# Kernel optimization log

Measured on AMD Instinct MI355X. Metric: run time of the kernel, lower is better.

## Reference

```python
import jax, jax.numpy as jnp
import numpy as np

B, T, S1, S2 = 4, 256, 256, 256
D = 512          # tgt_dims == src_dims
V = 32000        # tgt_voc_size
H, DH = 8, 64    # heads, head_dims; HID = H*DH == D
HID = H * DH
VEXT = V + S1 + S2


def layer_norm(x):
    m = jnp.mean(x, axis=-1, keepdims=True)
    v = jnp.mean((x - m) ** 2, axis=-1, keepdims=True)
    return (x - m) / jnp.sqrt(v + 1e-5)


def copy_attention(query, key, qmask, kmask, Wq, bq, Wk, bk, Wv, bv, Wo, bo):
    # conv1d with kernel 1 == linear; weights are [out, in]
    b, t, _ = query.shape
    s = key.shape[1]
    q = (query @ Wq.T + bq).reshape(b, t, H, DH).transpose(0, 2, 1, 3) * (DH ** -0.5)
    k = (key @ Wk.T + bk).reshape(b, s, H, DH).transpose(0, 2, 1, 3)
    v = (key @ Wv.T + bv).reshape(b, s, H, DH).transpose(0, 2, 1, 3)
    att = jnp.einsum('bhtd,bhkd->bhtk', q, k)            # [B,H,T,S]
    out_att = att * kmask[:, None, None, :]              # multiplicative mask copy
    att = jnp.where((kmask == 0)[:, None, None, :], -jnp.inf, att)
    att = jax.nn.softmax(att, axis=-1)
    out = jnp.einsum('bhtk,bhkd->bhtd', att, v)
    out = out.transpose(0, 2, 1, 3).reshape(b, t, HID)
    out = (out @ Wo.T + bo) * qmask[:, :, None]
    out_att = out_att * qmask[:, None, :, None]
    return out_att.mean(axis=1), out                     # [B,T,S], [B,T,D]


def scatter_copy(att, map_idx):
    # copy_output[b, t, map_idx[b, s]] += att[b, t, s]  (accumulate=True)
    b, t, s = att.shape
    bi = jnp.arange(b)[:, None, None]
    ti = jnp.arange(t)[None, :, None]
    out = jnp.zeros((b, t, VEXT), att.dtype)
    return out.at[bi, ti, map_idx[:, None, :]].add(att)


def setup_inputs() -> dict:
    key = jax.random.key(0)
    ks = jax.random.split(key, 24)
    p = 0.02
    inp = {
        'tgt_dec_out': jax.random.normal(ks[0], (B, T, D), jnp.float32),
        'src1_key': jax.random.normal(ks[1], (B, S1, D), jnp.float32),
        'src1_map_idx': jax.random.randint(ks[2], (B, S1), 0, VEXT),
        'src2_key': jax.random.normal(ks[3], (B, S2, D), jnp.float32),
        'src2_map_idx': jax.random.randint(ks[4], (B, S2), 0, VEXT),
        'Wfc': jax.random.normal(ks[5], (V, D), jnp.float32) * p,
        'bfc': jnp.zeros((V,), jnp.float32),
        'Wp': jax.random.normal(ks[6], (3, 3 * D), jnp.float32) * p,
        'bp': jnp.zeros((3,), jnp.float32),
    }
    i = 7
    for a in ('1', '2'):
        for nm in ('Wq', 'Wk', 'Wv', 'Wo'):
            inp[nm + a] = jax.random.normal(ks[i], (HID, D), jnp.float32) * p
            inp[nm.replace('W', 'b') + a] = jnp.zeros((HID,), jnp.float32)
            i += 1
    return inp


def reference(tgt_dec_out, src1_key, src1_map_idx, src2_key, src2_map_idx,
              Wfc, bfc, Wp, bp,
              Wq1, bq1, Wk1, bk1, Wv1, bv1, Wo1, bo1,
              Wq2, bq2, Wk2, bk2, Wv2, bv2, Wo2, bo2):
    tgt_output = layer_norm(tgt_dec_out @ Wfc.T + bfc)          # [B,T,V]
    tgt_output = jnp.pad(tgt_output, ((0, 0), (0, 0), (0, S1 + S2)))  # [B,T,VEXT]
    tgt_mask = jnp.sign(jnp.abs(tgt_dec_out).sum(-1))
    src1_mask = jnp.sign(jnp.abs(src1_key).sum(-1))
    src2_mask = jnp.sign(jnp.abs(src2_key).sum(-1))
    att1, c1 = copy_attention(tgt_dec_out, src1_key, tgt_mask, src1_mask,
                              Wq1, bq1, Wk1, bk1, Wv1, bv1, Wo1, bo1)
    copy1 = scatter_copy(layer_norm(att1), src1_map_idx)
    att2, c2 = copy_attention(tgt_dec_out, src2_key, tgt_mask, src2_mask,
                              Wq2, bq2, Wk2, bk2, Wv2, bv2, Wo2, bo2)
    copy2 = scatter_copy(layer_norm(att2), src2_map_idx)
    p = jax.nn.softmax(jnp.concatenate([tgt_dec_out, c1, c2], axis=-1) @ Wp.T + bp, axis=-1)  # [B,T,3]
    out = tgt_output * p[..., 0:1] + copy1 * p[..., 1:2] + copy2 * p[..., 2:3]
    return out
```

## Files before the change

kernel.cpp:

```cpp
#include <hip/hip_runtime.h>
#include <hip/hip_bf16.h>
#include <cstdint>
#include <cstddef>

#define B_     4
#define T_     256
#define S_     256
#define D_     512
#define V_     32000
#define H_     8
#define DH_    64
#define HID_   512
#define VEXT_  32512
#define BT_    1024
#define CHUNK_ 8192
#define NSEG_  23

typedef __hip_bfloat16 bf16;
typedef __bf16 bf16x8 __attribute__((ext_vector_type(8)));
typedef float  f32x4  __attribute__((ext_vector_type(4)));

__device__ inline void store_val(float* p, float v) { *p = v; }
__device__ inline void store_val(bf16* p, float v)  { *p = __float2bfloat16(v); }

__device__ inline float bfbits2f(unsigned short u) {
    return __uint_as_float(((unsigned)u) << 16);
}
__device__ inline unsigned short f2bfbits(float f) {
    bf16 h = __float2bfloat16(f);
    union { bf16 h; unsigned short u; } cv; cv.h = h; return cv.u;
}

__device__ __forceinline__ void glds16(const bf16* gsrc, bf16* ldst) {
    __builtin_amdgcn_global_load_lds(
        (const __attribute__((address_space(1))) unsigned int*)(gsrc),
        (__attribute__((address_space(3))) unsigned int*)(ldst),
        16, 0, 0);
}

__global__ void probe_kernel(const unsigned short* __restrict__ x, int* __restrict__ flag,
                             float* __restrict__ rsum, float* __restrict__ rsq)
{
    __shared__ int cnt;
    if (threadIdx.x == 0) cnt = 0;
    __syncthreads();
    for (int i = threadIdx.x; i < BT_; i += 256) { rsum[i] = 0.f; rsq[i] = 0.f; }
    int c = 0;
    for (int i = threadIdx.x; i < 4096; i += 256) {
        const int e = (x[i] >> 7) & 0xFF;
        if (e >= 96 && e <= 159) c++;
    }
    atomicAdd(&cnt, c);
    __syncthreads();
    if (threadIdx.x == 0) *flag = (cnt < 3500) ? 1 : 0;
}

struct ConvArgs {
    const void* src[NSEG_];
    void*       dst[NSEG_];
};

__global__ __launch_bounds__(256)
void convert_all_kernel(ConvArgs a, const int* __restrict__ flag)
{
    const int CNT[NSEG_] = {
        524288, 524288, 524288, 32000, 4608, 3,
        262144, 262144, 512, 512,
        262144, 262144, 512, 512,
        262144, 262144, 512, 512,
        262144, 512, 262144, 512,
        16384000
    };
    const int fm = *flag;
    int seg = 0, blk = blockIdx.x;
    for (;;) {
        const int nb = (CNT[seg] + 8191) >> 13;
        if (blk < nb) break;
        blk -= nb; seg++;
    }
    const int n    = CNT[seg];
    const int j0   = blk << 13;
    const int jend = (n < j0 + 8192) ? n : (j0 + 8192);
    if (fm) {
        const float* s = (const float*)a.src[seg];
        unsigned short* d = (unsigned short*)a.dst[seg];
        for (int j = j0 + threadIdx.x * 4; j < jend; j += 1024) {
            if (j + 4 <= jend) {
                float4 v = *(const float4*)(s + j);
                ushort4 u;
                u.x = f2bfbits(v.x); u.y = f2bfbits(v.y);
                u.z = f2bfbits(v.z); u.w = f2bfbits(v.w);
                *(ushort4*)(d + j) = u;
            } else {
                for (int t = j; t < jend; t++) d[t] = f2bfbits(s[t]);
            }
        }
    } else {
        const unsigned short* s = (const unsigned short*)a.src[seg];
        unsigned short* d = (unsigned short*)a.dst[seg];
        for (int j = j0 + threadIdx.x * 4; j < jend; j += 1024) {
            if (j + 4 <= jend) {
                *(ushort4*)(d + j) = *(const ushort4*)(s + j);
            } else {
                for (int t = j; t < jend; t++) d[t] = s[t];
            }
        }
    }
}

__global__ void masks_kernel(const bf16* __restrict__ tgt, const bf16* __restrict__ s1,
                             const bf16* __restrict__ s2, float* __restrict__ mt,
                             float* __restrict__ m1, float* __restrict__ m2)
{
    const int row = blockIdx.x;
    const bf16* src; float* dst;
    if (row < BT_)           { src = tgt + (size_t)row * D_;            dst = mt + row; }
    else if (row < 2 * BT_)  { src = s1 + (size_t)(row - BT_) * D_;     dst = m1 + (row - BT_); }
    else                     { src = s2 + (size_t)(row - 2 * BT_) * D_; dst = m2 + (row - 2 * BT_); }
    const int lane = threadIdx.x;
    float s = 0.f;
    for (int i = lane; i < D_; i += 64) s += fabsf(__bfloat162float(src[i]));
#pragma unroll
    for (int off = 32; off; off >>= 1) s += __shfl_down(s, off);
    if (lane == 0) *dst = (s > 0.f) ? 1.f : 0.f;
}

template <typename OutT>
__device__ __forceinline__
void gemm_tile_body(const bf16* __restrict__ A, const bf16* __restrict__ Bw,
                    const bf16* __restrict__ bias, OutT* __restrict__ C,
                    const int K, const int ldC, const int m0, const int n0,
                    bf16* As, bf16* Bs)
{
    const int tid  = threadIdx.x;
    const int lane = tid & 63;
    const int wave = tid >> 6;
    const int quad = lane >> 4, l16 = lane & 15;
    const int wm = (wave >> 1) * 64, wn = (wave & 1) * 64;

    f32x4 acc[4][4];
#pragma unroll
    for (int i = 0; i < 4; i++)
#pragma unroll
        for (int j = 0; j < 4; j++) acc[i][j] = (f32x4){0.f, 0.f, 0.f, 0.f};

    const int row0 = tid >> 2;
    const int kp   = (tid & 3) * 8;
    bf16* ldsA0 = As + wave * 512;
    bf16* ldsA1 = As + 2048 + wave * 512;
    bf16* ldsB0 = Bs + wave * 512;
    bf16* ldsB1 = Bs + 2048 + wave * 512;

    for (int k0 = 0; k0 < K; k0 += 32) {
        glds16(A  + (size_t)(m0 + row0)      * K + k0 + kp, ldsA0);
        glds16(A  + (size_t)(m0 + row0 + 64) * K + k0 + kp, ldsA1);
        glds16(Bw + (size_t)(n0 + row0)      * K + k0 + kp, ldsB0);
        glds16(Bw + (size_t)(n0 + row0 + 64) * K + k0 + kp, ldsB1);
        __syncthreads();

        bf16x8 af[4], bfv[4];
#pragma unroll
        for (int i = 0; i < 4; i++)
            af[i] = *(const bf16x8*)(As + (wm + i * 16 + l16) * 32 + quad * 8);
#pragma unroll
        for (int j = 0; j < 4; j++)
            bfv[j] = *(const bf16x8*)(Bs + (wn + j * 16 + l16) * 32 + quad * 8);
#pragma unroll
        for (int i = 0; i < 4; i++)
#pragma unroll
            for (int j = 0; j < 4; j++)
                acc[i][j] = __builtin_amdgcn_mfma_f32_16x16x32_bf16(af[i], bfv[j], acc[i][j], 0, 0, 0);
        __syncthreads();
    }

#pragma unroll
    for (int i = 0; i < 4; i++)
#pragma unroll
        for (int j = 0; j < 4; j++) {
            const int nb = n0 + wn + j * 16 + l16;
            const float bv = __bfloat162float(bias[nb]);
#pragma unroll
            for (int r = 0; r < 4; r++) {
                const int m = m0 + wm + i * 16 + quad * 4 + r;
                store_val(C + (size_t)m * ldC + nb, acc[i][j][r] + bv);
            }
        }
}

struct Proj3Args {
    const bf16* A[3];
    const bf16* W[3];
    const bf16* b[3];
    bf16*       C[3];
};

__global__ __launch_bounds__(256)
void gemm_proj3_kernel(Proj3Args pa)
{
    __shared__ bf16 As[128 * 32];
    __shared__ bf16 Bs[128 * 32];
    const int z = blockIdx.z;
    gemm_tile_body<bf16>(pa.A[z], pa.W[z], pa.b[z], pa.C[z], D_, 1024,
                         blockIdx.y * 128, blockIdx.x * 128, As, Bs);
}

struct Out2Args {
    const bf16* A[2];
    const bf16* W[2];
    const bf16* b[2];
    float*      C[2];
};

__global__ __launch_bounds__(256)
void gemm_out2_kernel(Out2Args oa)
{
    __shared__ bf16 As[128 * 32];
    __shared__ bf16 Bs[128 * 32];
    const int z = blockIdx.z;
    gemm_tile_body<float>(oa.A[z], oa.W[z], oa.b[z], oa.C[z], D_, HID_,
                          blockIdx.y * 128, blockIdx.x * 128, As, Bs);
}

__global__ __launch_bounds__(256)
void gemm_fc_kernel(const bf16* __restrict__ A, const bf16* __restrict__ Bw,
                    const bf16* __restrict__ bias, void* __restrict__ Cv,
                    const int* __restrict__ flag,
                    float* __restrict__ rsum, float* __restrict__ rsq)
{
    __shared__ bf16 As[128 * 32];
    __shared__ bf16 Bs[128 * 32];
    const int fm = *flag;
    const int tid  = threadIdx.x;
    const int lane = tid & 63;
    const int wave = tid >> 6;
    const int quad = lane >> 4, l16 = lane & 15;
    const int f  = (blockIdx.x & 7) * 250 + (blockIdx.x >> 3);
    const int m0 = (f & 7) * 128;
    const int n0 = (f >> 3) * 128;
    const int wm = (wave >> 1) * 64, wn = (wave & 1) * 64;

    f32x4 acc[4][4];
#pragma unroll
    for (int i = 0; i < 4; i++)
#pragma unroll
        for (int j = 0; j < 4; j++) acc[i][j] = (f32x4){0.f, 0.f, 0.f, 0.f};

    const int row0 = tid >> 2;
    const int kp   = (tid & 3) * 8;
    bf16* ldsA0 = As + wave * 512;
    bf16* ldsA1 = As + 2048 + wave * 512;
    bf16* ldsB0 = Bs + wave * 512;
    bf16* ldsB1 = Bs + 2048 + wave * 512;

    for (int k0 = 0; k0 < D_; k0 += 32) {
        glds16(A  + (size_t)(m0 + row0)      * D_ + k0 + kp, ldsA0);
        glds16(A  + (size_t)(m0 + row0 + 64) * D_ + k0 + kp, ldsA1);
        glds16(Bw + (size_t)(n0 + row0)      * D_ + k0 + kp, ldsB0);
        glds16(Bw + (size_t)(n0 + row0 + 64) * D_ + k0 + kp, ldsB1);
        __syncthreads();

        bf16x8 af[4], bfv[4];
#pragma unroll
        for (int i = 0; i < 4; i++)
            af[i] = *(const bf16x8*)(As + (wm + i * 16 + l16) * 32 + quad * 8);
#pragma unroll
        for (int j = 0; j < 4; j++)
            bfv[j] = *(const bf16x8*)(Bs + (wn + j * 16 + l16) * 32 + quad * 8);
#pragma unroll
        for (int i = 0; i < 4; i++)
#pragma unroll
            for (int j = 0; j < 4; j++)
                acc[i][j] = __builtin_amdgcn_mfma_f32_16x16x32_bf16(af[i], bfv[j], acc[i][j], 0, 0, 0);
        __syncthreads();
    }

    float srow[4][4], sqr[4][4];
#pragma unroll
    for (int i = 0; i < 4; i++)
#pragma unroll
        for (int r = 0; r < 4; r++) { srow[i][r] = 0.f; sqr[i][r] = 0.f; }

#pragma unroll
    for (int i = 0; i < 4; i++)
#pragma unroll
        for (int j = 0; j < 4; j++) {
            const int nb = n0 + wn + j * 16 + l16;
            const float bv = __bfloat162float(bias[nb]);
#pragma unroll
            for (int r = 0; r < 4; r++) {
                const int m = m0 + wm + i * 16 + quad * 4 + r;
                const float val = acc[i][j][r] + bv;
                if (fm) ((float*)Cv)[(size_t)m * VEXT_ + nb] = val;
                else    ((bf16*)Cv)[(size_t)m * VEXT_ + nb] = __float2bfloat16(val);
                srow[i][r] += val;
                sqr[i][r]  += val * val;
            }
        }

#pragma unroll
    for (int i = 0; i < 4; i++)
#pragma unroll
        for (int r = 0; r < 4; r++) {
            float s = srow[i][r], q = sqr[i][r];
#pragma unroll
            for (int off = 1; off <= 8; off <<= 1) {
                s += __shfl_xor(s, off);
                q += __shfl_xor(q, off);
            }
            if (l16 == 0) {
                const int m = m0 + wm + i * 16 + quad * 4 + r;
                atomicAdd(&rsum[m], s);
                atomicAdd(&rsq[m],  q);
            }
        }
}

__global__ __launch_bounds__(256)
void attn_qk_kernel(const bf16* __restrict__ qcat, const bf16* __restrict__ kv1,
                    const bf16* __restrict__ kv2, float* __restrict__ scores)
{
    __shared__ bf16 As[128 * 32];
    __shared__ bf16 Bs[128 * 32];
    const int tid  = threadIdx.x;
    const int lane = tid & 63;
    const int wave = tid >> 6;
    const int quad = lane >> 4, l16 = lane & 15;
    const int z = blockIdx.z;
    const int stream = z >> 5, b = (z >> 3) & 3, h = z & 7;
    const bf16* kv = stream ? kv2 : kv1;
    const int m0 = blockIdx.y * 128, n0 = blockIdx.x * 128;
    const int wm = (wave >> 1) * 64, wn = (wave & 1) * 64;

    f32x4 acc[4][4];
#pragma unroll
    for (int i = 0; i < 4; i++)
#pragma unroll
        for (int j = 0; j < 4; j++) acc[i][j] = (f32x4){0.f, 0.f, 0.f, 0.f};

    const int row0 = tid >> 2;
    const int kp   = (tid & 3) * 8;
    bf16* ldsA0 = As + wave * 512;
    bf16* ldsA1 = As + 2048 + wave * 512;
    bf16* ldsB0 = Bs + wave * 512;
    bf16* ldsB1 = Bs + 2048 + wave * 512;

    const bf16* Abase = qcat + (size_t)(b * 256) * 1024 + stream * 512 + h * 64;
    const bf16* Bbase = kv   + (size_t)(b * 256) * 1024 + h * 64;

    for (int k0 = 0; k0 < 64; k0 += 32) {
        glds16(Abase + (size_t)(m0 + row0)      * 1024 + k0 + kp, ldsA0);
        glds16(Abase + (size_t)(m0 + row0 + 64) * 1024 + k0 + kp, ldsA1);
        glds16(Bbase + (size_t)(n0 + row0)      * 1024 + k0 + kp, ldsB0);
        glds16(Bbase + (size_t)(n0 + row0 + 64) * 1024 + k0 + kp, ldsB1);
        __syncthreads();

        bf16x8 af[4], bfv[4];
#pragma unroll
        for (int i = 0; i < 4; i++)
            af[i] = *(const bf16x8*)(As + (wm + i * 16 + l16) * 32 + quad * 8);
#pragma unroll
        for (int j = 0; j < 4; j++)
            bfv[j] = *(const bf16x8*)(Bs + (wn + j * 16 + l16) * 32 + quad * 8);
#pragma unroll
        for (int i = 0; i < 4; i++)
#pragma unroll
            for (int j = 0; j < 4; j++)
                acc[i][j] = __builtin_amdgcn_mfma_f32_16x16x32_bf16(af[i], bfv[j], acc[i][j], 0, 0, 0);
        __syncthreads();
    }

    float* sp = scores + (size_t)z * 65536;
#pragma unroll
    for (int i = 0; i < 4; i++)
#pragma unroll
        for (int j = 0; j < 4; j++) {
            const int nb = n0 + wn + j * 16 + l16;
#pragma unroll
            for (int r = 0; r < 4; r++) {
                const int m = m0 + wm + i * 16 + quad * 4 + r;
                sp[(size_t)m * 256 + nb] = acc[i][j][r] * 0.125f;
            }
        }
}

__global__ __launch_bounds__(256)
void attn_sm_kernel(const float* __restrict__ scores,
                    const bf16* __restrict__ kv1, const bf16* __restrict__ kv2,
                    const float* __restrict__ qmask,
                    const float* __restrict__ km1, const float* __restrict__ km2,
                    bf16* __restrict__ ctx1, bf16* __restrict__ ctx2,
                    float* __restrict__ lno1, float* __restrict__ lno2)
{
    __shared__ float pvs[4][H_][260];
    const int y = blockIdx.y;
    const bf16* kv = y ? kv2 : kv1;
    const float* kmask = y ? km2 : km1;
    bf16* ctx = y ? ctx2 : ctx1;
    float* lnout = y ? lno2 : lno1;

    const int tid = threadIdx.x;
    const int lane = tid & 63, wv = tid >> 6;
    const int bt = blockIdx.x * 4 + wv;
    const int b  = bt >> 8, t = bt & 255;

    float kmv[4]; bool on[4];
#pragma unroll
    for (int i = 0; i < 4; i++) {
        kmv[i] = kmask[b * S_ + lane + 64 * i];
        on[i] = kmv[i] != 0.f;
    }

    const float* sbase = scores + (size_t)(y * 32 + b * 8) * 65536 + (size_t)t * 256;
    float msum[4] = {0.f, 0.f, 0.f, 0.f};

    for (int h = 0; h < H_; h++) {
        const float* sp = sbase + (size_t)h * 65536;
        float sc[4];
#pragma unroll
        for (int i = 0; i < 4; i++) sc[i] = sp[lane + 64 * i];

        float xs[4];
        float mx = -INFINITY;
#pragma unroll
        for (int i = 0; i < 4; i++) {
            msum[i] += sc[i];
            xs[i] = on[i] ? sc[i] : -INFINITY;
            mx = fmaxf(mx, xs[i]);
        }
#pragma unroll
        for (int off = 32; off; off >>= 1) mx = fmaxf(mx, __shfl_xor(mx, off));
        float e[4], ts = 0.f;
        const bool live = (mx > -INFINITY);
#pragma unroll
        for (int i = 0; i < 4; i++) {
            e[i] = (on[i] && live) ? __expf(xs[i] - mx) : 0.f;
            ts += e[i];
        }
#pragma unroll
        for (int off = 32; off; off >>= 1) ts += __shfl_xor(ts, off);
        const float inv = (ts > 0.f) ? 1.f / ts : 0.f;
#pragma unroll
        for (int i = 0; i < 4; i++)
            pvs[wv][h][lane + 64 * i] = e[i] * inv;
    }

    {
        const float* prow = pvs[wv][lane >> 3];
        const bf16* vp = kv + (size_t)(b * S_) * 1024 + 512 + lane * 8;
        float o0 = 0.f, o1 = 0.f, o2 = 0.f, o3 = 0.f, o4 = 0.f, o5 = 0.f, o6 = 0.f, o7 = 0.f;
#pragma unroll 8
        for (int s = 0; s < S_; s++) {
            ushort4 u0 = *(const ushort4*)(vp + (size_t)s * 1024);
            ushort4 u1 = *(const ushort4*)(vp + (size_t)s * 1024 + 4);
            const float pv = prow[s];
            o0 += pv * bfbits2f(u0.x); o1 += pv * bfbits2f(u0.y);
            o2 += pv * bfbits2f(u0.z); o3 += pv * bfbits2f(u0.w);
            o4 += pv * bfbits2f(u1.x); o5 += pv * bfbits2f(u1.y);
            o6 += pv * bfbits2f(u1.z); o7 += pv * bfbits2f(u1.w);
        }
        ushort4 w0, w1;
        w0.x = f2bfbits(o0); w0.y = f2bfbits(o1); w0.z = f2bfbits(o2); w0.w = f2bfbits(o3);
        w1.x = f2bfbits(o4); w1.y = f2bfbits(o5); w1.z = f2bfbits(o6); w1.w = f2bfbits(o7);
        bf16* cp = ctx + (size_t)bt * HID_ + lane * 8;
        *(ushort4*)(cp) = w0;
        *(ushort4*)(cp + 4) = w1;
    }

    const float qm = qmask[bt];
    float am[4], s1 = 0.f;
#pragma unroll
    for (int i = 0; i < 4; i++) {
        am[i] = msum[i] * (1.f / H_) * kmv[i] * qm;
        s1 += am[i];
    }
#pragma unroll
    for (int off = 32; off; off >>= 1) s1 += __shfl_xor(s1, off);
    const float mean = s1 * (1.f / S_);
    float dv = 0.f;
#pragma unroll
    for (int i = 0; i < 4; i++) dv += (am[i] - mean) * (am[i] - mean);
#pragma unroll
    for (int off = 32; off; off >>= 1) dv += __shfl_xor(dv, off);
    const float rstd = rsqrtf(fmaxf(dv * (1.f / S_), 0.f) + 1e-5f);
#pragma unroll
    for (int i = 0; i < 4; i++)
        lnout[(size_t)bt * S_ + lane + 64 * i] = (am[i] - mean) * rstd;
}

__global__ void pgate_kernel(const bf16* __restrict__ x, const float* __restrict__ c1,
                             const float* __restrict__ c2, const float* __restrict__ qmask,
                             const bf16* __restrict__ Wp, const bf16* __restrict__ bp,
                             float* __restrict__ p)
{
    const int bt = blockIdx.x;
    const int lane = threadIdx.x;
    const float qm = qmask[bt];
    float a0 = 0.f, a1 = 0.f, a2 = 0.f;
    for (int d = lane; d < D_; d += 64) {
        const float xv  = __bfloat162float(x[(size_t)bt * D_ + d]);
        const float c1v = c1[(size_t)bt * D_ + d] * qm;
        const float c2v = c2[(size_t)bt * D_ + d] * qm;
        a0 += xv * __bfloat162float(Wp[0 * 3 * D_ + d])
            + c1v * __bfloat162float(Wp[0 * 3 * D_ + D_ + d])
            + c2v * __bfloat162float(Wp[0 * 3 * D_ + 2 * D_ + d]);
        a1 += xv * __bfloat162float(Wp[1 * 3 * D_ + d])
            + c1v * __bfloat162float(Wp[1 * 3 * D_ + D_ + d])
            + c2v * __bfloat162float(Wp[1 * 3 * D_ + 2 * D_ + d]);
        a2 += xv * __bfloat162float(Wp[2 * 3 * D_ + d])
            + c1v * __bfloat162float(Wp[2 * 3 * D_ + D_ + d])
            + c2v * __bfloat162float(Wp[2 * 3 * D_ + 2 * D_ + d]);
    }
#pragma unroll
    for (int off = 32; off; off >>= 1) {
        a0 += __shfl_down(a0, off);
        a1 += __shfl_down(a1, off);
        a2 += __shfl_down(a2, off);
    }
    if (lane == 0) {
        float l0 = a0 + __bfloat162float(bp[0]);
        float l1 = a1 + __bfloat162float(bp[1]);
        float l2 = a2 + __bfloat162float(bp[2]);
        float mx = fmaxf(l0, fmaxf(l1, l2));
        float e0 = __expf(l0 - mx), e1 = __expf(l1 - mx), e2 = __expf(l2 - mx);
        float inv = 1.f / (e0 + e1 + e2);
        p[bt * 3 + 0] = e0 * inv; p[bt * 3 + 1] = e1 * inv; p[bt * 3 + 2] = e2 * inv;
    }
}

__global__ __launch_bounds__(256)
void final_kernel(void* __restrict__ outv, const int* __restrict__ flag,
                  const float* __restrict__ ln1, const float* __restrict__ ln2,
                  const int* __restrict__ map1, const int* __restrict__ map2,
                  const float* __restrict__ p,
                  const float* __restrict__ rsum, const float* __restrict__ rsq)
{
    __shared__ float chnk[CHUNK_];
    const int fm = *flag;
    const int bt = blockIdx.x, b = bt >> 8, tid = threadIdx.x;
    const float p0 = p[bt * 3], p1 = p[bt * 3 + 1], p2 = p[bt * 3 + 2];
    const float m = rsum[bt] * (1.f / V_);
    const float var = fmaxf(rsq[bt] * (1.f / V_) - m * m, 0.f);
    const float r = rsqrtf(var + 1e-5f);
    const size_t rbase = (size_t)bt * VEXT_;

    for (int c = 0; c < 4; c++) {
        const int jlo = c * CHUNK_;
        const int n = (VEXT_ - jlo < CHUNK_) ? (VEXT_ - jlo) : CHUNK_;
        for (int jj = tid * 4; jj < n; jj += 1024) {
            const int j = jlo + jj;
            float4 fv = {0.f, 0.f, 0.f, 0.f};
            if (j < V_) {
                float v0, v1, v2, v3;
                if (fm) {
                    float4 u = *(const float4*)((const float*)outv + rbase + j);
                    v0 = u.x; v1 = u.y; v2 = u.z; v3 = u.w;
                } else {
                    ushort4 u = *(const ushort4*)((const unsigned short*)outv + rbase + j);
                    v0 = bfbits2f(u.x); v1 = bfbits2f(u.y); v2 = bfbits2f(u.z); v3 = bfbits2f(u.w);
                }
                fv.x = p0 * (v0 - m) * r;
                fv.y = p0 * (v1 - m) * r;
                fv.z = p0 * (v2 - m) * r;
                fv.w = p0 * (v3 - m) * r;
            }
            *(float4*)(chnk + jj) = fv;
        }
        __syncthreads();
        for (int e = tid; e < 2 * S_; e += 256) {
            const int src = e >> 8, si = e & 255;
            const int j = (src ? map2 : map1)[b * S_ + si];
            if (j >= jlo && j < jlo + n) {
                const float val = (src ? p2 : p1) * (src ? ln2 : ln1)[(size_t)bt * S_ + si];
                atomicAdd(&chnk[j - jlo], val);
            }
        }
        __syncthreads();
        if (fm) {
            float* orow = (float*)outv + rbase;
            for (int jj = tid * 4; jj < n; jj += 1024)
                *(float4*)(orow + jlo + jj) = *(const float4*)(chnk + jj);
        } else {
            unsigned short* orow = (unsigned short*)outv + rbase;
            for (int jj = tid * 4; jj < n; jj += 1024) {
                float4 v = *(const float4*)(chnk + jj);
                ushort4 u;
                u.x = f2bfbits(v.x); u.y = f2bfbits(v.y); u.z = f2bfbits(v.z); u.w = f2bfbits(v.w);
                *(ushort4*)(orow + jlo + jj) = u;
            }
        }
        __syncthreads();
    }
}

extern "C" void kernel_launch(void* const* d_in, const int* in_sizes, int n_in,
                              void* d_out, int out_size, void* d_ws, size_t ws_size,
                              hipStream_t stream)
{
    const int* map1 = (const int*)d_in[2];
    const int* map2 = (const int*)d_in[4];

    char* w = (char*)d_ws;
    size_t off = 0;
    auto carve = [&](size_t bytes) -> char* {
        char* ptr = w + off;
        off = (off + bytes + 255) & ~(size_t)255;
        return ptr;
    };
    int* flag = (int*)carve(16);

    bf16* xc   = (bf16*)carve((size_t)BT_ * D_ * 2);
    bf16* s1c  = (bf16*)carve((size_t)B_ * S_ * D_ * 2);
    bf16* s2c  = (bf16*)carve((size_t)B_ * S_ * D_ * 2);
    bf16* Wfcc = (bf16*)carve((size_t)V_ * D_ * 2);
    bf16* bfcc = (bf16*)carve((size_t)V_ * 2);
    bf16* Wpc  = (bf16*)carve((size_t)3 * 3 * D_ * 2);
    bf16* bpc  = (bf16*)carve(3 * 2);
    bf16* Wqq  = (bf16*)carve((size_t)2 * HID_ * D_ * 2);
    bf16* bqq  = (bf16*)carve((size_t)2 * HID_ * 2);
    bf16* Wkv1 = (bf16*)carve((size_t)2 * HID_ * D_ * 2);
    bf16* bkv1 = (bf16*)carve((size_t)2 * HID_ * 2);
    bf16* Wkv2 = (bf16*)carve((size_t)2 * HID_ * D_ * 2);
    bf16* bkv2 = (bf16*)carve((size_t)2 * HID_ * 2);
    bf16* Wo1c = (bf16*)carve((size_t)HID_ * D_ * 2);
    bf16* bo1c = (bf16*)carve((size_t)HID_ * 2);
    bf16* Wo2c = (bf16*)carve((size_t)HID_ * D_ * 2);
    bf16* bo2c = (bf16*)carve((size_t)HID_ * 2);

    bf16*  qcat = (bf16*) carve((size_t)BT_ * 1024 * 2);
    bf16*  kv1  = (bf16*) carve((size_t)BT_ * 1024 * 2);
    bf16*  kv2  = (bf16*) carve((size_t)BT_ * 1024 * 2);
    bf16*  ctx1 = (bf16*) carve((size_t)BT_ * HID_ * 2);
    bf16*  ctx2 = (bf16*) carve((size_t)BT_ * HID_ * 2);
    float* c1   = (float*)carve((size_t)BT_ * HID_ * 4);
    float* c2   = (float*)carve((size_t)BT_ * HID_ * 4);
    float* ln1  = (float*)carve((size_t)BT_ * S_ * 4);
    float* ln2  = (float*)carve((size_t)BT_ * S_ * 4);
    float* p    = (float*)carve((size_t)BT_ * 3 * 4);
    float* mt   = (float*)carve((size_t)BT_ * 4);
    float* m1   = (float*)carve((size_t)BT_ * 4);
    float* m2   = (float*)carve((size_t)BT_ * 4);
    float* rsum = (float*)carve((size_t)BT_ * 4);
    float* rsq  = (float*)carve((size_t)BT_ * 4);
    float* scr  = (float*)carve((size_t)64 * 65536 * 4);
    (void)ws_size; (void)in_sizes; (void)n_in; (void)out_size;

    probe_kernel<<<1, 256, 0, stream>>>((const unsigned short*)d_in[0], flag, rsum, rsq);

    ConvArgs ca;
    ca.src[0]  = d_in[0];  ca.dst[0]  = xc;
    ca.src[1]  = d_in[1];  ca.dst[1]  = s1c;
    ca.src[2]  = d_in[3];  ca.dst[2]  = s2c;
    ca.src[3]  = d_in[6];  ca.dst[3]  = bfcc;
    ca.src[4]  = d_in[7];  ca.dst[4]  = Wpc;
    ca.src[5]  = d_in[8];  ca.dst[5]  = bpc;
    ca.src[6]  = d_in[9];  ca.dst[6]  = Wqq;
    ca.src[7]  = d_in[17]; ca.dst[7]  = Wqq + (size_t)HID_ * D_;
    ca.src[8]  = d_in[10]; ca.dst[8]  = bqq;
    ca.src[9]  = d_in[18]; ca.dst[9]  = bqq + HID_;
    ca.src[10] = d_in[11]; ca.dst[10] = Wkv1;
    ca.src[11] = d_in[13]; ca.dst[11] = Wkv1 + (size_t)HID_ * D_;
    ca.src[12] = d_in[12]; ca.dst[12] = bkv1;
    ca.src[13] = d_in[14]; ca.dst[13] = bkv1 + HID_;
    ca.src[14] = d_in[19]; ca.dst[14] = Wkv2;
    ca.src[15] = d_in[21]; ca.dst[15] = Wkv2 + (size_t)HID_ * D_;
    ca.src[16] = d_in[20]; ca.dst[16] = bkv2;
    ca.src[17] = d_in[22]; ca.dst[17] = bkv2 + HID_;
    ca.src[18] = d_in[15]; ca.dst[18] = Wo1c;
    ca.src[19] = d_in[16]; ca.dst[19] = bo1c;
    ca.src[20] = d_in[23]; ca.dst[20] = Wo2c;
    ca.src[21] = d_in[24]; ca.dst[21] = bo2c;
    ca.src[22] = d_in[5];  ca.dst[22] = Wfcc;
    convert_all_kernel<<<2462, 256, 0, stream>>>(ca, flag);

    masks_kernel<<<3 * BT_, 64, 0, stream>>>(xc, s1c, s2c, mt, m1, m2);

    gemm_fc_kernel<<<2000, 256, 0, stream>>>(xc, Wfcc, bfcc, d_out, flag, rsum, rsq);

    Proj3Args pa;
    pa.A[0] = xc;   pa.W[0] = Wqq;  pa.b[0] = bqq;  pa.C[0] = qcat;
    pa.A[1] = s1c;  pa.W[1] = Wkv1; pa.b[1] = bkv1; pa.C[1] = kv1;
    pa.A[2] = s2c;  pa.W[2] = Wkv2; pa.b[2] = bkv2; pa.C[2] = kv2;
    gemm_proj3_kernel<<<dim3(1024 / 128, BT_ / 128, 3), 256, 0, stream>>>(pa);

    attn_qk_kernel<<<dim3(2, 2, 64), 256, 0, stream>>>(qcat, kv1, kv2, scr);

    attn_sm_kernel<<<dim3(BT_ / 4, 2), 256, 0, stream>>>(scr, kv1, kv2, mt, m1, m2,
                                                         ctx1, ctx2, ln1, ln2);

    Out2Args oa;
    oa.A[0] = ctx1; oa.W[0] = Wo1c; oa.b[0] = bo1c; oa.C[0] = c1;
    oa.A[1] = ctx2; oa.W[1] = Wo2c; oa.b[1] = bo2c; oa.C[1] = c2;
    gemm_out2_kernel<<<dim3(HID_ / 128, BT_ / 128, 2), 256, 0, stream>>>(oa);

    pgate_kernel<<<BT_, 64, 0, stream>>>(xc, c1, c2, mt, Wpc, bpc, p);

    final_kernel<<<BT_, 256, 0, stream>>>(d_out, flag, ln1, ln2, map1, map2, p, rsum, rsq);
}
```

Before: 422.2 us.

## Double-buffer LDS in GEMM kernels and replace row-stat atomics with per-tile partials

All GEMM-style kernels switch to two LDS buffers, so the next K-slice is fetched with global_load_lds while MFMAs run on the current one. This removes one barrier per iteration but doubles LDS use per block, which may lower occupancy. The FC GEMM no longer issues global float atomics for layernorm row sums. Each tile instead writes its partial sums to a [250,1024] buffer, and the final kernel reduces them, which also removes the zeroing in the probe kernel. The FC grid changes from a swizzled 1D launch to a plain 2D (8,250) grid, which changes the block visit order and L2 reuse.

```diff
diff --git a/kernel.cpp b/kernel.cpp
--- a/kernel.cpp
+++ b/kernel.cpp
@@ -15,6 +15,7 @@
 #define BT_    1024
 #define CHUNK_ 8192
 #define NSEG_  23
+#define NT_    250
 
 typedef __hip_bfloat16 bf16;
 typedef __bf16 bf16x8 __attribute__((ext_vector_type(8)));
@@ -38,13 +39,11 @@
         16, 0, 0);
 }
 
-__global__ void probe_kernel(const unsigned short* __restrict__ x, int* __restrict__ flag,
-                             float* __restrict__ rsum, float* __restrict__ rsq)
+__global__ void probe_kernel(const unsigned short* __restrict__ x, int* __restrict__ flag)
 {
     __shared__ int cnt;
     if (threadIdx.x == 0) cnt = 0;
     __syncthreads();
-    for (int i = threadIdx.x; i < BT_; i += 256) { rsum[i] = 0.f; rsq[i] = 0.f; }
     int c = 0;
     for (int i = threadIdx.x; i < 4096; i += 256) {
         const int e = (x[i] >> 7) & 0xFF;
@@ -130,7 +129,7 @@
 void gemm_tile_body(const bf16* __restrict__ A, const bf16* __restrict__ Bw,
                     const bf16* __restrict__ bias, OutT* __restrict__ C,
                     const int K, const int ldC, const int m0, const int n0,
-                    bf16* As, bf16* Bs)
+                    bf16 (*As)[4096], bf16 (*Bs)[4096])
 {
     const int tid  = threadIdx.x;
     const int lane = tid & 63;
@@ -146,31 +145,35 @@
 
     const int row0 = tid >> 2;
     const int kp   = (tid & 3) * 8;
-    bf16* ldsA0 = As + wave * 512;
-    bf16* ldsA1 = As + 2048 + wave * 512;
-    bf16* ldsB0 = Bs + wave * 512;
-    bf16* ldsB1 = Bs + 2048 + wave * 512;
-
-    for (int k0 = 0; k0 < K; k0 += 32) {
-        glds16(A  + (size_t)(m0 + row0)      * K + k0 + kp, ldsA0);
-        glds16(A  + (size_t)(m0 + row0 + 64) * K + k0 + kp, ldsA1);
-        glds16(Bw + (size_t)(n0 + row0)      * K + k0 + kp, ldsB0);
-        glds16(Bw + (size_t)(n0 + row0 + 64) * K + k0 + kp, ldsB1);
-        __syncthreads();
+    const int nk   = K >> 5;
+
+    auto stage = [&](int buf, int k0) {
+        glds16(A  + (size_t)(m0 + row0)      * K + k0 + kp, As[buf] + wave * 512);
+        glds16(A  + (size_t)(m0 + row0 + 64) * K + k0 + kp, As[buf] + 2048 + wave * 512);
+        glds16(Bw + (size_t)(n0 + row0)      * K + k0 + kp, Bs[buf] + wave * 512);
+        glds16(Bw + (size_t)(n0 + row0 + 64) * K + k0 + kp, Bs[buf] + 2048 + wave * 512);
+    };
+
+    stage(0, 0);
+    __syncthreads();
+    int cur = 0;
+    for (int ks = 0; ks < nk; ks++) {
+        if (ks + 1 < nk) stage(cur ^ 1, (ks + 1) * 32);
 
         bf16x8 af[4], bfv[4];
 #pragma unroll
         for (int i = 0; i < 4; i++)
-            af[i] = *(const bf16x8*)(As + (wm + i * 16 + l16) * 32 + quad * 8);
+            af[i] = *(const bf16x8*)(As[cur] + (wm + i * 16 + l16) * 32 + quad * 8);
 #pragma unroll
         for (int j = 0; j < 4; j++)
-            bfv[j] = *(const bf16x8*)(Bs + (wn + j * 16 + l16) * 32 + quad * 8);
+            bfv[j] = *(const bf16x8*)(Bs[cur] + (wn + j * 16 + l16) * 32 + quad * 8);
 #pragma unroll
         for (int i = 0; i < 4; i++)
 #pragma unroll
             for (int j = 0; j < 4; j++)
                 acc[i][j] = __builtin_amdgcn_mfma_f32_16x16x32_bf16(af[i], bfv[j], acc[i][j], 0, 0, 0);
-        __syncthreads();
+
+        if (ks + 1 < nk) { __syncthreads(); cur ^= 1; }
     }
 
 #pragma unroll
@@ -197,8 +200,8 @@
 __global__ __launch_bounds__(256)
 void gemm_proj3_kernel(Proj3Args pa)
 {
-    __shared__ bf16 As[128 * 32];
-    __shared__ bf16 Bs[128 * 32];
+    __shared__ bf16 As[2][4096];
+    __shared__ bf16 Bs[2][4096];
     const int z = blockIdx.z;
     gemm_tile_body<bf16>(pa.A[z], pa.W[z], pa.b[z], pa.C[z], D_, 1024,
                          blockIdx.y * 128, blockIdx.x * 128, As, Bs);
@@ -214,8 +217,8 @@
 __global__ __launch_bounds__(256)
 void gemm_out2_kernel(Out2Args oa)
 {
-    __shared__ bf16 As[128 * 32];
-    __shared__ bf16 Bs[128 * 32];
+    __shared__ bf16 As[2][4096];
+    __shared__ bf16 Bs[2][4096];
     const int z = blockIdx.z;
     gemm_tile_body<float>(oa.A[z], oa.W[z], oa.b[z], oa.C[z], D_, HID_,
                           blockIdx.y * 128, blockIdx.x * 128, As, Bs);
@@ -225,18 +228,19 @@
 void gemm_fc_kernel(const bf16* __restrict__ A, const bf16* __restrict__ Bw,
                     const bf16* __restrict__ bias, void* __restrict__ Cv,
                     const int* __restrict__ flag,
-                    float* __restrict__ rsum, float* __restrict__ rsq)
-{
-    __shared__ bf16 As[128 * 32];
-    __shared__ bf16 Bs[128 * 32];
+                    float* __restrict__ psum, float* __restrict__ psq)
+{
+    __shared__ bf16 As[2][4096];
+    __shared__ bf16 Bs[2][4096];
+    __shared__ float sred[128], qred[128];
     const int fm = *flag;
     const int tid  = threadIdx.x;
     const int lane = tid & 63;
     const int wave = tid >> 6;
     const int quad = lane >> 4, l16 = lane & 15;
-    const int f  = (blockIdx.x & 7) * 250 + (blockIdx.x >> 3);
-    const int m0 = (f & 7) * 128;
-    const int n0 = (f >> 3) * 128;
+    const int m0 = blockIdx.x * 128;
+    const int nt = blockIdx.y;
+    const int n0 = nt * 128;
     const int wm = (wave >> 1) * 64, wn = (wave & 1) * 64;
 
     f32x4 acc[4][4];
@@ -247,31 +251,34 @@
 
     const int row0 = tid >> 2;
     const int kp   = (tid & 3) * 8;
-    bf16* ldsA0 = As + wave * 512;
-    bf16* ldsA1 = As + 2048 + wave * 512;
-    bf16* ldsB0 = Bs + wave * 512;
-    bf16* ldsB1 = Bs + 2048 + wave * 512;
-
-    for (int k0 = 0; k0 < D_; k0 += 32) {
-        glds16(A  + (size_t)(m0 + row0)      * D_ + k0 + kp, ldsA0);
-        glds16(A  + (size_t)(m0 + row0 + 64) * D_ + k0 + kp, ldsA1);
-        glds16(Bw + (size_t)(n0 + row0)      * D_ + k0 + kp, ldsB0);
-        glds16(Bw + (size_t)(n0 + row0 + 64) * D_ + k0 + kp, ldsB1);
-        __syncthreads();
+
+    auto stage = [&](int buf, int k0) {
+        glds16(A  + (size_t)(m0 + row0)      * D_ + k0 + kp, As[buf] + wave * 512);
+        glds16(A  + (size_t)(m0 + row0 + 64) * D_ + k0 + kp, As[buf] + 2048 + wave * 512);
+        glds16(Bw + (size_t)(n0 + row0)      * D_ + k0 + kp, Bs[buf] + wave * 512);
+        glds16(Bw + (size_t)(n0 + row0 + 64) * D_ + k0 + kp, Bs[buf] + 2048 + wave * 512);
+    };
+
+    stage(0, 0);
+    __syncthreads();
+    int cur = 0;
+    for (int ks = 0; ks < 16; ks++) {
+        if (ks + 1 < 16) stage(cur ^ 1, (ks + 1) * 32);
 
         bf16x8 af[4], bfv[4];
 #pragma unroll
         for (int i = 0; i < 4; i++)
-            af[i] = *(const bf16x8*)(As + (wm + i * 16 + l16) * 32 + quad * 8);
+            af[i] = *(const bf16x8*)(As[cur] + (wm + i * 16 + l16) * 32 + quad * 8);
 #pragma unroll
         for (int j = 0; j < 4; j++)
-            bfv[j] = *(const bf16x8*)(Bs + (wn + j * 16 + l16) * 32 + quad * 8);
+            bfv[j] = *(const bf16x8*)(Bs[cur] + (wn + j * 16 + l16) * 32 + quad * 8);
 #pragma unroll
         for (int i = 0; i < 4; i++)
 #pragma unroll
             for (int j = 0; j < 4; j++)
                 acc[i][j] = __builtin_amdgcn_mfma_f32_16x16x32_bf16(af[i], bfv[j], acc[i][j], 0, 0, 0);
-        __syncthreads();
+
+        if (ks + 1 < 16) { __syncthreads(); cur ^= 1; }
     }
 
     float srow[4][4], sqr[4][4];
@@ -307,20 +314,39 @@
                 s += __shfl_xor(s, off);
                 q += __shfl_xor(q, off);
             }
-            if (l16 == 0) {
-                const int m = m0 + wm + i * 16 + quad * 4 + r;
-                atomicAdd(&rsum[m], s);
-                atomicAdd(&rsq[m],  q);
-            }
-        }
+            srow[i][r] = s; sqr[i][r] = q;
+        }
+    __syncthreads();
+    if (wn == 0) {
+#pragma unroll
+        for (int i = 0; i < 4; i++)
+#pragma unroll
+            for (int r = 0; r < 4; r++)
+                if (l16 == 0) {
+                    const int ml = wm + i * 16 + quad * 4 + r;
+                    sred[ml] = srow[i][r]; qred[ml] = sqr[i][r];
+                }
+    }
+    __syncthreads();
+    if (wn == 64) {
+#pragma unroll
+        for (int i = 0; i < 4; i++)
+#pragma unroll
+            for (int r = 0; r < 4; r++)
+                if (l16 == 0) {
+                    const int ml = wm + i * 16 + quad * 4 + r;
+                    psum[(size_t)nt * BT_ + m0 + ml] = srow[i][r] + sred[ml];
+                    psq [(size_t)nt * BT_ + m0 + ml] = sqr[i][r] + qred[ml];
+                }
+    }
 }
 
 __global__ __launch_bounds__(256)
 void attn_qk_kernel(const bf16* __restrict__ qcat, const bf16* __restrict__ kv1,
                     const bf16* __restrict__ kv2, float* __restrict__ scores)
 {
-    __shared__ bf16 As[128 * 32];
-    __shared__ bf16 Bs[128 * 32];
+    __shared__ bf16 As[2][4096];
+    __shared__ bf16 Bs[2][4096];
     const int tid  = threadIdx.x;
     const int lane = tid & 63;
     const int wave = tid >> 6;
@@ -339,34 +365,37 @@
 
     const int row0 = tid >> 2;
     const int kp   = (tid & 3) * 8;
-    bf16* ldsA0 = As + wave * 512;
-    bf16* ldsA1 = As + 2048 + wave * 512;
-    bf16* ldsB0 = Bs + wave * 512;
-    bf16* ldsB1 = Bs + 2048 + wave * 512;
 
     const bf16* Abase = qcat + (size_t)(b * 256) * 1024 + stream * 512 + h * 64;
     const bf16* Bbase = kv   + (size_t)(b * 256) * 1024 + h * 64;
 
-    for (int k0 = 0; k0 < 64; k0 += 32) {
-        glds16(Abase + (size_t)(m0 + row0)      * 1024 + k0 + kp, ldsA0);
-        glds16(Abase + (size_t)(m0 + row0 + 64) * 1024 + k0 + kp, ldsA1);
-        glds16(Bbase + (size_t)(n0 + row0)      * 1024 + k0 + kp, ldsB0);
-        glds16(Bbase + (size_t)(n0 + row0 + 64) * 1024 + k0 + kp, ldsB1);
-        __syncthreads();
+    auto stage = [&](int buf, int k0) {
+        glds16(Abase + (size_t)(m0 + row0)      * 1024 + k0 + kp, As[buf] + wave * 512);
+        glds16(Abase + (size_t)(m0 + row0 + 64) * 1024 + k0 + kp, As[buf] + 2048 + wave * 512);
+        glds16(Bbase + (size_t)(n0 + row0)      * 1024 + k0 + kp, Bs[buf] + wave * 512);
+        glds16(Bbase + (size_t)(n0 + row0 + 64) * 1024 + k0 + kp, Bs[buf] + 2048 + wave * 512);
+    };
+
+    stage(0, 0);
+    __syncthreads();
+    int cur = 0;
+    for (int ks = 0; ks < 2; ks++) {
+        if (ks + 1 < 2) stage(cur ^ 1, 32);
 
         bf16x8 af[4], bfv[4];
 #pragma unroll
         for (int i = 0; i < 4; i++)
-            af[i] = *(const bf16x8*)(As + (wm + i * 16 + l16) * 32 + quad * 8);
+            af[i] = *(const bf16x8*)(As[cur] + (wm + i * 16 + l16) * 32 + quad * 8);
 #pragma unroll
         for (int j = 0; j < 4; j++)
-            bfv[j] = *(const bf16x8*)(Bs + (wn + j * 16 + l16) * 32 + quad * 8);
+            bfv[j] = *(const bf16x8*)(Bs[cur] + (wn + j * 16 + l16) * 32 + quad * 8);
 #pragma unroll
         for (int i = 0; i < 4; i++)
 #pragma unroll
             for (int j = 0; j < 4; j++)
                 acc[i][j] = __builtin_amdgcn_mfma_f32_16x16x32_bf16(af[i], bfv[j], acc[i][j], 0, 0, 0);
-        __syncthreads();
+
+        if (ks + 1 < 2) { __syncthreads(); cur ^= 1; }
     }
 
     float* sp = scores + (size_t)z * 65536;
@@ -532,14 +561,25 @@
                   const float* __restrict__ ln1, const float* __restrict__ ln2,
                   const int* __restrict__ map1, const int* __restrict__ map2,
                   const float* __restrict__ p,
-                  const float* __restrict__ rsum, const float* __restrict__ rsq)
+                  const float* __restrict__ psum, const float* __restrict__ psq)
 {
     __shared__ float chnk[CHUNK_];
+    __shared__ float rr[8];
     const int fm = *flag;
     const int bt = blockIdx.x, b = bt >> 8, tid = threadIdx.x;
+    const int lane = tid & 63, wv = tid >> 6;
     const float p0 = p[bt * 3], p1 = p[bt * 3 + 1], p2 = p[bt * 3 + 2];
-    const float m = rsum[bt] * (1.f / V_);
-    const float var = fmaxf(rsq[bt] * (1.f / V_) - m * m, 0.f);
+
+    float s = 0.f, q = 0.f;
+    if (tid < NT_) { s = psum[(size_t)tid * BT_ + bt]; q = psq[(size_t)tid * BT_ + bt]; }
+#pragma unroll
+    for (int off = 32; off; off >>= 1) { s += __shfl_down(s, off); q += __shfl_down(q, off); }
+    if (lane == 0) { rr[wv] = s; rr[4 + wv] = q; }
+    __syncthreads();
+    const float S = rr[0] + rr[1] + rr[2] + rr[3];
+    const float Q = rr[4] + rr[5] + rr[6] + rr[7];
+    const float m = S * (1.f / V_);
+    const float var = fmaxf(Q * (1.f / V_) - m * m, 0.f);
     const float r = rsqrtf(var + 1e-5f);
     const size_t rbase = (size_t)bt * VEXT_;
 
@@ -639,12 +679,12 @@
     float* mt   = (float*)carve((size_t)BT_ * 4);
     float* m1   = (float*)carve((size_t)BT_ * 4);
     float* m2   = (float*)carve((size_t)BT_ * 4);
-    float* rsum = (float*)carve((size_t)BT_ * 4);
-    float* rsq  = (float*)carve((size_t)BT_ * 4);
+    float* psum = (float*)carve((size_t)NT_ * BT_ * 4);
+    float* psq  = (float*)carve((size_t)NT_ * BT_ * 4);
     float* scr  = (float*)carve((size_t)64 * 65536 * 4);
     (void)ws_size; (void)in_sizes; (void)n_in; (void)out_size;
 
-    probe_kernel<<<1, 256, 0, stream>>>((const unsigned short*)d_in[0], flag, rsum, rsq);
+    probe_kernel<<<1, 256, 0, stream>>>((const unsigned short*)d_in[0], flag);
 
     ConvArgs ca;
     ca.src[0]  = d_in[0];  ca.dst[0]  = xc;
@@ -674,7 +714,7 @@
 
     masks_kernel<<<3 * BT_, 64, 0, stream>>>(xc, s1c, s2c, mt, m1, m2);
 
-    gemm_fc_kernel<<<2000, 256, 0, stream>>>(xc, Wfcc, bfcc, d_out, flag, rsum, rsq);
+    gemm_fc_kernel<<<dim3(8, NT_), 256, 0, stream>>>(xc, Wfcc, bfcc, d_out, flag, psum, psq);
 
     Proj3Args pa;
     pa.A[0] = xc;   pa.W[0] = Wqq;  pa.b[0] = bqq;  pa.C[0] = qcat;
@@ -694,5 +734,5 @@
 
     pgate_kernel<<<BT_, 64, 0, stream>>>(xc, c1, c2, mt, Wpc, bpc, p);
 
-    final_kernel<<<BT_, 256, 0, stream>>>(d_out, flag, ln1, ln2, map1, map2, p, rsum, rsq);
-}
+    final_kernel<<<BT_, 256, 0, stream>>>(d_out, flag, ln1, ln2, map1, map2, p, psum, psq);
+}
```

Measured after the change: 420.9 us. Within noise of the previous version (-0.3%).
